# Kernel optimization log

Hardware: AMD Instinct MI355X
Metric: run time of the kernel (lower is better)

Reference implementation:

```python
import jax, jax.numpy as jnp
import numpy as np

OUT_H, OUT_W = 512, 512  # from init_kwargs output_size


def _coords(out_size, in_size):
    # Half-pixel mapping matching the Triton kernel (align_corners=False,
    # source coordinate clamped at 0 like torch's bilinear interpolate).
    scale = in_size / out_size
    src = jnp.maximum((jnp.arange(out_size, dtype=jnp.float32) + 0.5) * scale - 0.5, 0.0)
    lo = jnp.clip(jnp.floor(src).astype(jnp.int32), 0, in_size - 1)
    hi = jnp.minimum(lo + 1, in_size - 1)
    frac = src - lo.astype(jnp.float32)
    return lo, hi, frac


def setup_inputs() -> dict:
    key = jax.random.key(0)
    x = jax.random.normal(key, (8, 256, 256, 64), dtype=jnp.float32)  # BHWC
    return {"x": x}


def reference(x):
    b, in_h, in_w, c = x.shape
    y0, y1, dy = _coords(OUT_H, in_h)  # [OUT_H]
    x0, x1, dx = _coords(OUT_W, in_w)  # [OUT_W]

    # Gather the 4 neighbors: advanced indexing broadcasts (OUT_H,1)x(1,OUT_W)
    lt = x[:, y0[:, None], x0[None, :], :]  # [B, OUT_H, OUT_W, C]
    rt = x[:, y0[:, None], x1[None, :], :]
    lb = x[:, y1[:, None], x0[None, :], :]
    rb = x[:, y1[:, None], x1[None, :], :]

    dy_ = dy[None, :, None, None]
    dx_ = dx[None, None, :, None]
    out = (lt * (1 - dx_) * (1 - dy_)
           + rt * dx_ * (1 - dy_)
           + lb * (1 - dx_) * dy_
           + rb * dx_ * dy_)
    return out.astype(x.dtype)
```

## Files before the change

### kernel.cpp

```cpp
#include <hip/hip_runtime.h>


constexpr int B     = 8;
constexpr int IN_H  = 256;
constexpr int IN_W  = 256;
constexpr int OUT_H = 512;
constexpr int OUT_W = 512;
constexpr int C     = 64;
constexpr int C4    = C / 4;
constexpr int TOTAL = B * OUT_H * OUT_W * C4;

__global__ __launch_bounds__(256) void
bilerp2x_kernel(const float4* __restrict__ in, float4* __restrict__ out) {
    int i = blockIdx.x * blockDim.x + threadIdx.x;

    int c4   = i & (C4 - 1);
    int pix  = i >> 4;
    int ox   = pix & (OUT_W - 1);
    int rest = pix >> 9;
    int oy   = rest & (OUT_H - 1);
    int b    = rest >> 9;

    float sy = fmaxf((oy + 0.5f) * 0.5f - 0.5f, 0.0f);
    float sx = fmaxf((ox + 0.5f) * 0.5f - 0.5f, 0.0f);
    int y0 = (int)sy;
    int x0 = (int)sx;
    int y1 = min(y0 + 1, IN_H - 1);
    int x1 = min(x0 + 1, IN_W - 1);
    float dy = sy - (float)y0;
    float dx = sx - (float)x0;

    int row0 = (b * IN_H + y0) * IN_W;
    int row1 = (b * IN_H + y1) * IN_W;

    const float4 lt = in[(row0 + x0) * C4 + c4];
    const float4 rt = in[(row0 + x1) * C4 + c4];
    const float4 lb = in[(row1 + x0) * C4 + c4];
    const float4 rb = in[(row1 + x1) * C4 + c4];

    float4 t, bo, o;
    t.x = fmaf(dx, rt.x - lt.x, lt.x);
    t.y = fmaf(dx, rt.y - lt.y, lt.y);
    t.z = fmaf(dx, rt.z - lt.z, lt.z);
    t.w = fmaf(dx, rt.w - lt.w, lt.w);
    bo.x = fmaf(dx, rb.x - lb.x, lb.x);
    bo.y = fmaf(dx, rb.y - lb.y, lb.y);
    bo.z = fmaf(dx, rb.z - lb.z, lb.z);
    bo.w = fmaf(dx, rb.w - lb.w, lb.w);
    o.x = fmaf(dy, bo.x - t.x, t.x);
    o.y = fmaf(dy, bo.y - t.y, t.y);
    o.z = fmaf(dy, bo.z - t.z, t.z);
    o.w = fmaf(dy, bo.w - t.w, t.w);

    out[i] = o;
}

extern "C" void kernel_launch(void* const* d_in, const int* in_sizes, int n_in,
                              void* d_out, int out_size, void* d_ws, size_t ws_size,
                              hipStream_t stream) {
    (void)in_sizes; (void)n_in; (void)d_ws; (void)ws_size; (void)out_size;
    const float4* in  = (const float4*)d_in[0];
    float4*       out = (float4*)d_out;
    dim3 block(256);
    dim3 grid(TOTAL / 256);
    bilerp2x_kernel<<<grid, block, 0, stream>>>(in, out);
}
```

Measured before the change: 641.2 us.

## Compute two output rows per input row pair with nontemporal stores

Each thread now handles one pair of adjacent input rows and writes the two output rows that fall between them (dy of 0.25 and 0.75). The horizontal interpolation is shared, which halves the number of threads and the gather loads per output. It also adds a block-index swizzle and nontemporal stores to cut cache pollution from the large output. Edge rows are handled specially: row 0 is copied from the top interpolation, and the last pair skips its second row.

```diff
diff --git a/kernel.cpp b/kernel.cpp
--- a/kernel.cpp
+++ b/kernel.cpp
@@ -6,62 +6,69 @@
 constexpr int IN_W  = 256;
 constexpr int OUT_H = 512;
 constexpr int OUT_W = 512;
-constexpr int C     = 64;
-constexpr int C4    = C / 4;
-constexpr int TOTAL = B * OUT_H * OUT_W * C4;
+constexpr int C4    = 16;
+constexpr int TOTAL = B * IN_H * OUT_W * C4;
+
+typedef float v4f __attribute__((ext_vector_type(4)));
+
+static __device__ __forceinline__ v4f vfma(float a, v4f x, v4f y) {
+    v4f r;
+    r.x = fmaf(a, x.x, y.x);
+    r.y = fmaf(a, x.y, y.y);
+    r.z = fmaf(a, x.z, y.z);
+    r.w = fmaf(a, x.w, y.w);
+    return r;
+}
 
 __global__ __launch_bounds__(256) void
-bilerp2x_kernel(const float4* __restrict__ in, float4* __restrict__ out) {
-    int i = blockIdx.x * blockDim.x + threadIdx.x;
+bilerp2x_rowpair(const v4f* __restrict__ in, v4f* __restrict__ out) {
+    int bid = (int)blockIdx.x;
+    int swz = (bid & 7) * ((int)gridDim.x >> 3) + (bid >> 3);
+    int i   = swz * 256 + (int)threadIdx.x;
 
-    int c4   = i & (C4 - 1);
-    int pix  = i >> 4;
-    int ox   = pix & (OUT_W - 1);
-    int rest = pix >> 9;
-    int oy   = rest & (OUT_H - 1);
-    int b    = rest >> 9;
+    int c4 = i & (C4 - 1);
+    int r1 = i >> 4;
+    int ox = r1 & (OUT_W - 1);
+    int r2 = r1 >> 9;
+    int k  = r2 & (IN_H - 1);
+    int b  = r2 >> 8;
 
-    float sy = fmaxf((oy + 0.5f) * 0.5f - 0.5f, 0.0f);
     float sx = fmaxf((ox + 0.5f) * 0.5f - 0.5f, 0.0f);
-    int y0 = (int)sy;
-    int x0 = (int)sx;
-    int y1 = min(y0 + 1, IN_H - 1);
-    int x1 = min(x0 + 1, IN_W - 1);
-    float dy = sy - (float)y0;
+    int   x0 = (int)sx;
+    int   x1 = min(x0 + 1, IN_W - 1);
     float dx = sx - (float)x0;
 
-    int row0 = (b * IN_H + y0) * IN_W;
+    int y1   = min(k + 1, IN_H - 1);
+    int row0 = (b * IN_H + k)  * IN_W;
     int row1 = (b * IN_H + y1) * IN_W;
 
-    const float4 lt = in[(row0 + x0) * C4 + c4];
-    const float4 rt = in[(row0 + x1) * C4 + c4];
-    const float4 lb = in[(row1 + x0) * C4 + c4];
-    const float4 rb = in[(row1 + x1) * C4 + c4];
+    v4f lt = in[(row0 + x0) * C4 + c4];
+    v4f rt = in[(row0 + x1) * C4 + c4];
+    v4f lb = in[(row1 + x0) * C4 + c4];
+    v4f rb = in[(row1 + x1) * C4 + c4];
 
-    float4 t, bo, o;
-    t.x = fmaf(dx, rt.x - lt.x, lt.x);
-    t.y = fmaf(dx, rt.y - lt.y, lt.y);
-    t.z = fmaf(dx, rt.z - lt.z, lt.z);
-    t.w = fmaf(dx, rt.w - lt.w, lt.w);
-    bo.x = fmaf(dx, rb.x - lb.x, lb.x);
-    bo.y = fmaf(dx, rb.y - lb.y, lb.y);
-    bo.z = fmaf(dx, rb.z - lb.z, lb.z);
-    bo.w = fmaf(dx, rb.w - lb.w, lb.w);
-    o.x = fmaf(dy, bo.x - t.x, t.x);
-    o.y = fmaf(dy, bo.y - t.y, t.y);
-    o.z = fmaf(dy, bo.z - t.z, t.z);
-    o.w = fmaf(dy, bo.w - t.w, t.w);
+    v4f t  = vfma(dx, rt - lt, lt);
+    v4f bo = vfma(dx, rb - lb, lb);
+    v4f d  = bo - t;
+    v4f o1 = vfma(0.25f, d, t);
+    v4f o2 = vfma(0.75f, d, t);
 
-    out[i] = o;
+    int out_r1 = ((b * OUT_H + (2 * k + 1)) * OUT_W + ox) * C4 + c4;
+
+    __builtin_nontemporal_store(o1, &out[out_r1]);
+    if (k < IN_H - 1)
+        __builtin_nontemporal_store(o2, &out[out_r1 + OUT_W * C4]);
+    if (k == 0)
+        __builtin_nontemporal_store(t, &out[out_r1 - OUT_W * C4]);
 }
 
 extern "C" void kernel_launch(void* const* d_in, const int* in_sizes, int n_in,
                               void* d_out, int out_size, void* d_ws, size_t ws_size,
                               hipStream_t stream) {
     (void)in_sizes; (void)n_in; (void)d_ws; (void)ws_size; (void)out_size;
-    const float4* in  = (const float4*)d_in[0];
-    float4*       out = (float4*)d_out;
+    const v4f* in  = (const v4f*)d_in[0];
+    v4f*       out = (v4f*)d_out;
     dim3 block(256);
     dim3 grid(TOTAL / 256);
-    bilerp2x_kernel<<<grid, block, 0, stream>>>(in, out);
+    bilerp2x_rowpair<<<grid, block, 0, stream>>>(in, out);
 }
```

Measured after the change: 635.5 us. No clear change (-0.9%).
